# Kernel optimization log

Measured on AMD Instinct MI355X. Metric: run time of the kernel, lower is better.

## Reference

```python
import jax, jax.numpy as jnp
import numpy as np

EPS = 1e-8


def setup_inputs() -> dict:
    key = jax.random.key(0)
    k1, k2 = jax.random.split(key)
    a = jax.random.normal(k1, (1, 256, 128, 128), dtype=jnp.float32)
    b = jax.random.normal(k2, (1, 256, 128, 128), dtype=jnp.float32)
    return {"a": a, "b": b}


def reference(a, b):
    # a: [n, c, h, w] rendered feats; b: [n, c, h2, w2] style feats (n == 1)
    n, c, h, w = a.shape
    a_flat = a.reshape(n, c, -1)            # [n, c, hw]
    b_flat = b.reshape(n, c, -1)            # [n, c, h2w2]

    # argmin_cos_distance: channel-wise L2 normalize, cosine distance, argmin
    b_norm = jnp.sqrt((b_flat * b_flat).sum(1, keepdims=True) + EPS)
    b_n = b_flat / (b_norm + EPS)
    a_norm = jnp.sqrt((a_flat * a_flat).sum(1, keepdims=True) + EPS)
    a_n = a_flat / (a_norm + EPS)
    d_mat = 1.0 - jnp.einsum('ncp,ncq->npq', a_n, b_n)   # [n, hw, h2w2]
    z_best = jnp.argmin(d_mat, axis=2)                    # [n, hw]

    # nn_feat_replace: gather matched (unnormalized) style features
    idx = jnp.broadcast_to(z_best[:, None, :], b_flat.shape)
    target = jnp.take_along_axis(b_flat, idx, axis=2).reshape(n, c, h, w)

    # cos_loss(a, target): cosine distance over channel dim, mean over pixels
    an = jnp.sqrt((a * a).sum(1, keepdims=True))
    tn = jnp.sqrt((target * target).sum(1, keepdims=True))
    cossim = ((a / (an + EPS)) * (target / (tn + EPS))).sum(1)  # [n, h, w]
    return (1.0 - cossim).mean()
```

## Files before the change

kernel.cpp:

```cpp
#include <hip/hip_runtime.h>
#include <stdint.h>

#define EPS 1e-8f

constexpr int HW = 16384;
constexpr int BM = 128;
constexpr int NG = 2048;

typedef __attribute__((ext_vector_type(4))) float floatx4;
typedef __attribute__((ext_vector_type(4))) int   intx4;
typedef __attribute__((ext_vector_type(8))) int   intx8;
typedef unsigned char u8;
typedef unsigned int u32;
typedef unsigned long long u64;

typedef const __attribute__((address_space(1))) u32 gas_u32;
typedef __attribute__((address_space(3))) u32 las_u32;
__device__ inline void stage16(const void* g, void* l) {
    __builtin_amdgcn_global_load_lds((gas_u32*)g, (las_u32*)l, 16, 0, 0);
}

__device__ inline u32 pk4(float x0, float x1, float x2, float x3) {
    int t = __builtin_amdgcn_cvt_pk_fp8_f32(x0, x1, 0, false);
    t = __builtin_amdgcn_cvt_pk_fp8_f32(x2, x3, t, true);
    return (u32)t;
}

__global__ __launch_bounds__(512) void prep_kernel(const float* __restrict__ a,
                                                   const float* __restrict__ b,
                                                   float* __restrict__ sumsq_a,
                                                   float* __restrict__ sumsq_b,
                                                   u8* __restrict__ aF, u8* __restrict__ bF,
                                                   u64* __restrict__ packed,
                                                   float* __restrict__ out) {
    __shared__ float red[16][33];
    __shared__ float invb_sh[32];
    const int tid = threadIdx.x;
    const int px = tid & 31, cu = tid >> 5;
    const int p0 = blockIdx.x * 32;
    const int p = p0 + px;
    const int c0 = cu * 16;
    const u32 g = (u32)(p >> 4), r = (u32)(p & 15);
    const u32 sbase = g * 4096u + (u32)(cu >> 3) * 2048u + (u32)(cu & 1) * 1024u
                    + ((u32)((cu >> 1) & 3) * 16u + r) * 16u;

    if (blockIdx.x < 32) packed[(size_t)blockIdx.x * 512 + tid] = 0ull;
    if (blockIdx.x == 0 && tid == 0) *out = 0.f;

    float bv[16];
    float s = 0.f;
    #pragma unroll
    for (int e = 0; e < 16; ++e) {
        bv[e] = b[(size_t)(c0 + e) * HW + p];
        s += bv[e] * bv[e];
    }
    red[cu][px] = s;
    __syncthreads();
    if (tid < 32) {
        float B = 0.f;
        #pragma unroll
        for (int j = 0; j < 16; ++j) B += red[j][tid];
        sumsq_b[p0 + tid] = B;
        invb_sh[tid] = 1.0f / (sqrtf(B + EPS) + EPS);
    }
    __syncthreads();

    {
        const float inv = invb_sh[px];
        int4 W;
        W.x = (int)pk4(bv[0] * inv, bv[1] * inv, bv[2] * inv, bv[3] * inv);
        W.y = (int)pk4(bv[4] * inv, bv[5] * inv, bv[6] * inv, bv[7] * inv);
        W.z = (int)pk4(bv[8] * inv, bv[9] * inv, bv[10] * inv, bv[11] * inv);
        W.w = (int)pk4(bv[12] * inv, bv[13] * inv, bv[14] * inv, bv[15] * inv);
        *(int4*)(bF + sbase) = W;
    }

    {
        float av[16];
        s = 0.f;
        #pragma unroll
        for (int e = 0; e < 16; ++e) {
            av[e] = a[(size_t)(c0 + e) * HW + p];
            s += av[e] * av[e];
        }
        int4 W;
        W.x = (int)pk4(av[0], av[1], av[2], av[3]);
        W.y = (int)pk4(av[4], av[5], av[6], av[7]);
        W.z = (int)pk4(av[8], av[9], av[10], av[11]);
        W.w = (int)pk4(av[12], av[13], av[14], av[15]);
        *(int4*)(aF + sbase) = W;
    }
    red[cu][px] = s;
    __syncthreads();
    if (tid < 32) {
        float A = 0.f;
        #pragma unroll
        for (int j = 0; j < 16; ++j) A += red[j][tid];
        sumsq_a[p0 + tid] = A;
    }
}

__global__ __launch_bounds__(256, 3) void gemm_argmax(const u8* __restrict__ aF,
                                                      const u8* __restrict__ bF,
                                                      u64* __restrict__ packed) {
    __shared__ u8 sB[2][16384];
    const int tid = threadIdx.x;
    const int w = tid >> 6, lane = tid & 63;
    const int q4 = lane >> 4, r15 = lane & 15;
    const int wm = w >> 1, wn = w & 1;

    const u32 bid = blockIdx.x;
    const u32 ng = bid & 7;
    const u32 mt = bid >> 3;
    const int p0 = (int)mt * BM;

    const u8* gA = aF + (((size_t)(mt * 8 + wm * 4)) << 12) + (u32)lane * 16;
    intx8 Afr[4][2];
    #pragma unroll
    for (int mi = 0; mi < 4; ++mi)
        #pragma unroll
        for (int kb = 0; kb < 2; ++kb)
            Afr[mi][kb] = __builtin_shufflevector(
                *(const intx4*)(gA + (u32)(mi * 4096 + kb * 2048)),
                *(const intx4*)(gA + (u32)(mi * 4096 + kb * 2048 + 1024)),
                0, 1, 2, 3, 4, 5, 6, 7);

    const u8* gQ = bF + ((size_t)ng << 19);
    const u32 so = (u32)w * 4096u + (u32)lane * 16u;

    #pragma unroll
    for (int i = 0; i < 4; ++i)
        stage16(gQ + so + (u32)(i * 1024), &sB[0][w * 4096 + i * 1024]);

    float bestv[4][4];
    u32   bestq[4][4];
    #pragma unroll
    for (int mi = 0; mi < 4; ++mi)
        #pragma unroll
        for (int r = 0; r < 4; ++r) { bestv[mi][r] = -3.4e38f; bestq[mi][r] = 0; }

    u32 q0 = ng * 2048 + wn * 32 + (u32)r15;
    const floatx4 C64 = {64.f, 64.f, 64.f, 64.f};
    const int SCL = 0x7F7F7F7F;

    __syncthreads();

    int x = 0;
    for (int qt = 0; qt < 32; ++qt) {
        if (qt < 31) {
            const u8* gs = gQ + (u32)(qt + 1) * 16384u + so;
            u8* ls = &sB[x ^ 1][w * 4096];
            #pragma unroll
            for (int i = 0; i < 4; ++i)
                stage16(gs + (u32)(i * 1024), ls + i * 1024);
        }

        const u8* Lb = &sB[x][(u32)(wn * 2) * 4096u + (u32)lane * 16u];
        floatx4 acc[4][2];
        intx8 B0, B1;

        { intx4 lo = *(const intx4*)(Lb);
          intx4 hi = *(const intx4*)(Lb + 1024);
          B0 = __builtin_shufflevector(lo, hi, 0, 1, 2, 3, 4, 5, 6, 7); }
        { intx4 lo = *(const intx4*)(Lb + 4096);
          intx4 hi = *(const intx4*)(Lb + 4096 + 1024);
          B1 = __builtin_shufflevector(lo, hi, 0, 1, 2, 3, 4, 5, 6, 7); }
        __builtin_amdgcn_s_setprio(1);
        #pragma unroll
        for (int mi = 0; mi < 4; ++mi)
            acc[mi][0] = __builtin_amdgcn_mfma_scale_f32_16x16x128_f8f6f4(
                Afr[mi][0], B0, C64, 0, 0, 0, SCL, 0, SCL);
        #pragma unroll
        for (int mi = 0; mi < 4; ++mi)
            acc[mi][1] = __builtin_amdgcn_mfma_scale_f32_16x16x128_f8f6f4(
                Afr[mi][0], B1, C64, 0, 0, 0, SCL, 0, SCL);
        __builtin_amdgcn_s_setprio(0);

        { intx4 lo = *(const intx4*)(Lb + 2048);
          intx4 hi = *(const intx4*)(Lb + 2048 + 1024);
          B0 = __builtin_shufflevector(lo, hi, 0, 1, 2, 3, 4, 5, 6, 7); }
        { intx4 lo = *(const intx4*)(Lb + 4096 + 2048);
          intx4 hi = *(const intx4*)(Lb + 4096 + 2048 + 1024);
          B1 = __builtin_shufflevector(lo, hi, 0, 1, 2, 3, 4, 5, 6, 7); }
        __builtin_amdgcn_s_setprio(1);
        #pragma unroll
        for (int mi = 0; mi < 4; ++mi)
            acc[mi][0] = __builtin_amdgcn_mfma_scale_f32_16x16x128_f8f6f4(
                Afr[mi][1], B0, acc[mi][0], 0, 0, 0, SCL, 0, SCL);
        #pragma unroll
        for (int mi = 0; mi < 4; ++mi)
            acc[mi][1] = __builtin_amdgcn_mfma_scale_f32_16x16x128_f8f6f4(
                Afr[mi][1], B1, acc[mi][1], 0, 0, 0, SCL, 0, SCL);
        __builtin_amdgcn_s_setprio(0);

        #pragma unroll
        for (int mi = 0; mi < 4; ++mi)
            #pragma unroll
            for (int r = 0; r < 4; ++r) {
                float v = acc[mi][0][r];
                bool gt = v > bestv[mi][r];
                bestv[mi][r] = gt ? v : bestv[mi][r];
                bestq[mi][r] = gt ? q0 : bestq[mi][r];
            }
        #pragma unroll
        for (int mi = 0; mi < 4; ++mi)
            #pragma unroll
            for (int r = 0; r < 4; ++r) {
                float v = acc[mi][1][r];
                bool gt = v > bestv[mi][r];
                bestv[mi][r] = gt ? v : bestv[mi][r];
                bestq[mi][r] = gt ? (q0 + 16u) : bestq[mi][r];
            }
        q0 += 64u;

        __syncthreads();
        x ^= 1;
    }

    #pragma unroll
    for (int mi = 0; mi < 4; ++mi)
        #pragma unroll
        for (int r = 0; r < 4; ++r) {
            u64 pk = ((u64)__float_as_uint(bestv[mi][r]) << 32)
                   | (u64)(0xFFFFFFFFu - bestq[mi][r]);
            #pragma unroll
            for (int d = 1; d < 16; d <<= 1) {
                u64 o = __shfl_xor((unsigned long long)pk, d);
                pk = o > pk ? o : pk;
            }
            if (r15 == 0)
                atomicMax(&packed[p0 + wm * 64 + mi * 16 + q4 * 4 + r], pk);
        }
}

__global__ void loss_kernel(const u64* __restrict__ packed,
                            const float* __restrict__ sumsq_a, const float* __restrict__ sumsq_b,
                            float* __restrict__ out) {
    int p = blockIdx.x * 256 + threadIdx.x;
    u64 pk = packed[p];
    float s = __uint_as_float((u32)(pk >> 32)) - 64.0f;
    u32 q = 0xFFFFFFFFu - (u32)(pk & 0xFFFFFFFFull);
    float A = sumsq_a[p], B = sumsq_b[q];
    float dot = s * (sqrtf(B + EPS) + EPS);
    float cossim = dot / ((sqrtf(A) + EPS) * (sqrtf(B) + EPS));
    float v = (1.0f - cossim) * (1.0f / (float)HW);
    #pragma unroll
    for (int d = 1; d < 64; d <<= 1) v += __shfl_xor(v, d);
    if ((threadIdx.x & 63) == 0) atomicAdd(out, v);
}

extern "C" void kernel_launch(void* const* d_in, const int* in_sizes, int n_in,
                              void* d_out, int out_size, void* d_ws, size_t ws_size,
                              hipStream_t stream) {
    const float* a = (const float*)d_in[0];
    const float* b = (const float*)d_in[1];
    float* out = (float*)d_out;
    char* ws = (char*)d_ws;

    u8*    aF      = (u8*)ws;
    u8*    bF      = (u8*)(ws + (size_t)4 * 1024 * 1024);
    float* sumsq_a = (float*)(ws + (size_t)8 * 1024 * 1024);
    float* sumsq_b = sumsq_a + HW;
    u64*   packed  = (u64*)(sumsq_b + HW);

    prep_kernel<<<dim3(HW / 32), 512, 0, stream>>>(a, b, sumsq_a, sumsq_b, aF, bF, packed, out);
    gemm_argmax<<<dim3((HW / BM) * (HW / NG)), 256, 0, stream>>>(aF, bF, packed);
    loss_kernel<<<dim3(HW / 256), 256, 0, stream>>>(packed, sumsq_a, sumsq_b, out);
}
```

Baseline: 141.4 us.

## Software-pipeline GEMM tiles so argmax overlaps next tile's MFMAs

The main loop is restructured to use two accumulator sets and is manually unrolled by two. The MFMAs for tile qt+1 are issued before the argmax compare/select on tile qt's results, so VALU argmax work can overlap matrix-core latency instead of waiting on it serially. The B-tile staging and barriers are re-sequenced to match the double-buffered LDS. The cost is a second set of 32 accumulator registers, which under the 3-block launch bound may raise register pressure or cause spills.

```diff
diff --git a/kernel.cpp b/kernel.cpp
--- a/kernel.cpp
+++ b/kernel.cpp
@@ -100,6 +100,62 @@
     }
 }
 
+#define MFMA1(A_, B_, C_) __builtin_amdgcn_mfma_scale_f32_16x16x128_f8f6f4( \
+        (A_), (B_), (C_), 0, 0, 0, SCL, 0, SCL)
+
+#define LDB(off_) __builtin_shufflevector(                                  \
+        *(const intx4*)(Lb + (off_)), *(const intx4*)(Lb + (off_) + 1024),  \
+        0, 1, 2, 3, 4, 5, 6, 7)
+
+#define MFMA_QT(acc_, buf_) do {                                            \
+    const u8* Lb = &sB[buf_][(u32)(wn * 2) * 4096u + (u32)lane * 16u];      \
+    intx8 Bk0n0 = LDB(0);                                                   \
+    intx8 Bk0n1 = LDB(4096);                                                \
+    __builtin_amdgcn_s_setprio(1);                                          \
+    _Pragma("unroll")                                                       \
+    for (int mi = 0; mi < 4; ++mi) {                                        \
+        acc_[mi][0] = MFMA1(Afr[mi][0], Bk0n0, C64);                        \
+        acc_[mi][1] = MFMA1(Afr[mi][0], Bk0n1, C64);                        \
+    }                                                                       \
+    __builtin_amdgcn_s_setprio(0);                                          \
+    intx8 Bk1n0 = LDB(2048);                                                \
+    intx8 Bk1n1 = LDB(4096 + 2048);                                         \
+    __builtin_amdgcn_s_setprio(1);                                          \
+    _Pragma("unroll")                                                       \
+    for (int mi = 0; mi < 4; ++mi) {                                        \
+        acc_[mi][0] = MFMA1(Afr[mi][1], Bk1n0, acc_[mi][0]);                \
+        acc_[mi][1] = MFMA1(Afr[mi][1], Bk1n1, acc_[mi][1]);                \
+    }                                                                       \
+    __builtin_amdgcn_s_setprio(0);                                          \
+} while (0)
+
+#define ARGMAX_QT(acc_, qt_) do {                                           \
+    const u32 qb_ = qbase + (u32)(qt_) * 64u;                               \
+    _Pragma("unroll")                                                       \
+    for (int mi = 0; mi < 4; ++mi) {                                        \
+        _Pragma("unroll")                                                   \
+        for (int ni = 0; ni < 2; ++ni) {                                    \
+            const u32 qc_ = qb_ + (u32)(ni * 16);                           \
+            _Pragma("unroll")                                               \
+            for (int rr = 0; rr < 4; ++rr) {                                \
+                float v_ = acc_[mi][ni][rr];                                \
+                bool gt_ = v_ > bestv[mi][rr];                              \
+                bestv[mi][rr] = gt_ ? v_ : bestv[mi][rr];                   \
+                bestq[mi][rr] = gt_ ? qc_ : bestq[mi][rr];                  \
+            }                                                               \
+        }                                                                   \
+    }                                                                       \
+} while (0)
+
+#define STAGE(buf_, qt_) do {                                               \
+    const u8* gs_ = gQ + (u32)(qt_) * 16384u + so;                          \
+    u8* ls_ = &sB[buf_][w * 4096];                                          \
+    stage16(gs_,        ls_);                                               \
+    stage16(gs_ + 1024, ls_ + 1024);                                        \
+    stage16(gs_ + 2048, ls_ + 2048);                                        \
+    stage16(gs_ + 3072, ls_ + 3072);                                        \
+} while (0)
+
 __global__ __launch_bounds__(256, 3) void gemm_argmax(const u8* __restrict__ aF,
                                                       const u8* __restrict__ bF,
                                                       u64* __restrict__ packed) {
@@ -128,108 +184,56 @@
     const u8* gQ = bF + ((size_t)ng << 19);
     const u32 so = (u32)w * 4096u + (u32)lane * 16u;
 
-    #pragma unroll
-    for (int i = 0; i < 4; ++i)
-        stage16(gQ + so + (u32)(i * 1024), &sB[0][w * 4096 + i * 1024]);
-
     float bestv[4][4];
     u32   bestq[4][4];
     #pragma unroll
     for (int mi = 0; mi < 4; ++mi)
         #pragma unroll
-        for (int r = 0; r < 4; ++r) { bestv[mi][r] = -3.4e38f; bestq[mi][r] = 0; }
-
-    u32 q0 = ng * 2048 + wn * 32 + (u32)r15;
+        for (int rr = 0; rr < 4; ++rr) { bestv[mi][rr] = -3.4e38f; bestq[mi][rr] = 0; }
+
+    const u32 qbase = ng * 2048 + wn * 32 + (u32)r15;
     const floatx4 C64 = {64.f, 64.f, 64.f, 64.f};
     const int SCL = 0x7F7F7F7F;
 
-    __syncthreads();
-
-    int x = 0;
-    for (int qt = 0; qt < 32; ++qt) {
-        if (qt < 31) {
-            const u8* gs = gQ + (u32)(qt + 1) * 16384u + so;
-            u8* ls = &sB[x ^ 1][w * 4096];
-            #pragma unroll
-            for (int i = 0; i < 4; ++i)
-                stage16(gs + (u32)(i * 1024), ls + i * 1024);
+    floatx4 accA[4][2], accB[4][2];
+
+    STAGE(0, 0);
+    __syncthreads();
+
+    STAGE(1, 1);
+    MFMA_QT(accA, 0);
+    __syncthreads();
+
+    for (int e = 0; e < 32; e += 2) {
+        const int o = e + 1;
+        if (o + 1 < 32) STAGE(0, o + 1);
+        MFMA_QT(accB, 1);
+        ARGMAX_QT(accA, e);
+        __syncthreads();
+
+        if (o + 1 < 32) {
+            STAGE(1, o + 2);
+            MFMA_QT(accA, 0);
+            ARGMAX_QT(accB, o);
+            __syncthreads();
+        } else {
+            ARGMAX_QT(accB, o);
         }
-
-        const u8* Lb = &sB[x][(u32)(wn * 2) * 4096u + (u32)lane * 16u];
-        floatx4 acc[4][2];
-        intx8 B0, B1;
-
-        { intx4 lo = *(const intx4*)(Lb);
-          intx4 hi = *(const intx4*)(Lb + 1024);
-          B0 = __builtin_shufflevector(lo, hi, 0, 1, 2, 3, 4, 5, 6, 7); }
-        { intx4 lo = *(const intx4*)(Lb + 4096);
-          intx4 hi = *(const intx4*)(Lb + 4096 + 1024);
-          B1 = __builtin_shufflevector(lo, hi, 0, 1, 2, 3, 4, 5, 6, 7); }
-        __builtin_amdgcn_s_setprio(1);
-        #pragma unroll
-        for (int mi = 0; mi < 4; ++mi)
-            acc[mi][0] = __builtin_amdgcn_mfma_scale_f32_16x16x128_f8f6f4(
-                Afr[mi][0], B0, C64, 0, 0, 0, SCL, 0, SCL);
-        #pragma unroll
-        for (int mi = 0; mi < 4; ++mi)
-            acc[mi][1] = __builtin_amdgcn_mfma_scale_f32_16x16x128_f8f6f4(
-                Afr[mi][0], B1, C64, 0, 0, 0, SCL, 0, SCL);
-        __builtin_amdgcn_s_setprio(0);
-
-        { intx4 lo = *(const intx4*)(Lb + 2048);
-          intx4 hi = *(const intx4*)(Lb + 2048 + 1024);
-          B0 = __builtin_shufflevector(lo, hi, 0, 1, 2, 3, 4, 5, 6, 7); }
-        { intx4 lo = *(const intx4*)(Lb + 4096 + 2048);
-          intx4 hi = *(const intx4*)(Lb + 4096 + 2048 + 1024);
-          B1 = __builtin_shufflevector(lo, hi, 0, 1, 2, 3, 4, 5, 6, 7); }
-        __builtin_amdgcn_s_setprio(1);
-        #pragma unroll
-        for (int mi = 0; mi < 4; ++mi)
-            acc[mi][0] = __builtin_amdgcn_mfma_scale_f32_16x16x128_f8f6f4(
-                Afr[mi][1], B0, acc[mi][0], 0, 0, 0, SCL, 0, SCL);
-        #pragma unroll
-        for (int mi = 0; mi < 4; ++mi)
-            acc[mi][1] = __builtin_amdgcn_mfma_scale_f32_16x16x128_f8f6f4(
-                Afr[mi][1], B1, acc[mi][1], 0, 0, 0, SCL, 0, SCL);
-        __builtin_amdgcn_s_setprio(0);
-
-        #pragma unroll
-        for (int mi = 0; mi < 4; ++mi)
-            #pragma unroll
-            for (int r = 0; r < 4; ++r) {
-                float v = acc[mi][0][r];
-                bool gt = v > bestv[mi][r];
-                bestv[mi][r] = gt ? v : bestv[mi][r];
-                bestq[mi][r] = gt ? q0 : bestq[mi][r];
-            }
-        #pragma unroll
-        for (int mi = 0; mi < 4; ++mi)
-            #pragma unroll
-            for (int r = 0; r < 4; ++r) {
-                float v = acc[mi][1][r];
-                bool gt = v > bestv[mi][r];
-                bestv[mi][r] = gt ? v : bestv[mi][r];
-                bestq[mi][r] = gt ? (q0 + 16u) : bestq[mi][r];
-            }
-        q0 += 64u;
-
-        __syncthreads();
-        x ^= 1;
     }
 
     #pragma unroll
     for (int mi = 0; mi < 4; ++mi)
         #pragma unroll
-        for (int r = 0; r < 4; ++r) {
-            u64 pk = ((u64)__float_as_uint(bestv[mi][r]) << 32)
-                   | (u64)(0xFFFFFFFFu - bestq[mi][r]);
+        for (int rr = 0; rr < 4; ++rr) {
+            u64 pk = ((u64)__float_as_uint(bestv[mi][rr]) << 32)
+                   | (u64)(0xFFFFFFFFu - bestq[mi][rr]);
             #pragma unroll
             for (int d = 1; d < 16; d <<= 1) {
-                u64 o = __shfl_xor((unsigned long long)pk, d);
-                pk = o > pk ? o : pk;
+                u64 oV = __shfl_xor((unsigned long long)pk, d);
+                pk = oV > pk ? oV : pk;
             }
             if (r15 == 0)
-                atomicMax(&packed[p0 + wm * 64 + mi * 16 + q4 * 4 + r], pk);
+                atomicMax(&packed[p0 + wm * 64 + mi * 16 + q4 * 4 + rr], pk);
         }
 }
 
```

New measurement: 294.8 us. 2.08x slower.
